# Optimization experiments

Measured on AMD Instinct MI355X. Metric: run time of the kernel, lower is better.

## Reference

```python
import jax, jax.numpy as jnp
import numpy as np

SIZE = 5   # local window side
HEADS = 1

def patch_extract(x, size):
    # x: [B, C, H, W] -> [B, C, size*size, H, W], replicate padding,
    # window index l = i*size + j (row-major over kernel), matching F.unfold.
    p = size // 2
    xp = jnp.pad(x, ((0, 0), (0, 0), (p, p), (p, p)), mode='edge')
    H, W = x.shape[2], x.shape[3]
    windows = [xp[:, :, i:i + H, j:j + W] for i in range(size) for j in range(size)]
    return jnp.stack(windows, axis=2)

def setup_inputs() -> dict:
    key = jax.random.key(0)
    k1, k2, k3, k4 = jax.random.split(key, 4)
    B, C, H, W = 4, 128, 64, 128
    attn = jax.random.normal(k1, (B, HEADS, H * W, SIZE * SIZE), dtype=jnp.float32)
    fmap = jax.random.normal(k2, (B, C, H, W), dtype=jnp.float32)
    Wv = jax.random.normal(k3, (C, C), dtype=jnp.float32) * (1.0 / np.sqrt(C))
    gamma = jax.random.normal(k4, (1,), dtype=jnp.float32)
    return {"attn": attn, "fmap": fmap, "Wv": Wv, "gamma": gamma}

def reference(attn, fmap, Wv, gamma):
    B, C, H, W = fmap.shape
    d = C // HEADS
    L = SIZE * SIZE
    # to_v: 1x1 conv, no bias
    v = jnp.einsum('oc,bchw->bohw', Wv, fmap)
    # local window gather: [B, C, L, H, W]
    v = patch_extract(v, SIZE)
    # 'b (h d) l x y -> b h (x y) d l'
    v = v.reshape(B, HEADS, d, L, H, W)
    v = v.transpose(0, 1, 4, 5, 2, 3).reshape(B, HEADS, H * W, d, L)
    # weighted sum over the local window
    out = jnp.einsum('bhnl,bhndl->bhnd', attn, v)
    # 'b h (x y) d -> b (h d) x y'
    out = out.reshape(B, HEADS, H, W, d).transpose(0, 1, 4, 2, 3).reshape(B, C, H, W)
    return fmap + gamma[0] * out
```

## Files before the change

kernel.cpp:

```cpp
#include <hip/hip_runtime.h>


namespace {
constexpr int Bn = 4, Cn = 128, Hn = 64, Wn = 128, Ln = 25;
constexpr int HWn = Hn * Wn;

constexpr int TY = 4, TX = 16;
constexpr int HY = 8, HX = 24;
constexpr int RS = 136;
constexpr int SVS = 136;
constexpr int WVS = 136;

typedef __attribute__((ext_vector_type(8))) short short8;
typedef __attribute__((ext_vector_type(4))) float f32x4;

__device__ inline unsigned short f2bf(float f) {
    unsigned u = __float_as_uint(f);
    return (unsigned short)((u + 0x7fffu + ((u >> 16) & 1u)) >> 16);
}

__global__ __launch_bounds__(256) void lsa_fused(
    const float* __restrict__ attn, const float* __restrict__ fmap,
    const float* __restrict__ Wv, const float* __restrict__ gamma,
    float* __restrict__ out)
{
    __shared__ alignas(16) unsigned short hs[HY * HX * RS];
    __shared__ alignas(16) unsigned short sv[TY * TX * SVS];
    __shared__ float at_s[TY * TX * Ln];

    const int tid = threadIdx.x;
    const int b = blockIdx.z;
    const int x0 = blockIdx.x * TX;
    const int y0 = blockIdx.y * TY;

    for (int i = tid; i < HY * 64 * 6; i += 256) {
        const int k = i % 6;
        const int r = i / 6;
        const int cp = r & 63;
        const int dy = r >> 6;
        const int ry = min(max(y0 + dy - 2, 0), Hn - 1);
        const int gxb = x0 - 4 + 4 * k;
        const size_t rowb = ((size_t)(b * Cn + 2 * cp)) * HWn + (size_t)ry * Wn;
        float4 va, vb;
        if (gxb < 0) {
            const float s0 = fmap[rowb], s1 = fmap[rowb + HWn];
            va.x = va.y = va.z = va.w = s0;
            vb.x = vb.y = vb.z = vb.w = s1;
        } else if (gxb > Wn - 4) {
            const float s0 = fmap[rowb + Wn - 1], s1 = fmap[rowb + HWn + Wn - 1];
            va.x = va.y = va.z = va.w = s0;
            vb.x = vb.y = vb.z = vb.w = s1;
        } else {
            va = *(const float4*)&fmap[rowb + gxb];
            vb = *(const float4*)&fmap[rowb + HWn + gxb];
        }
        unsigned short* hbase = &hs[(dy * HX + 4 * k) * RS + 2 * cp];
        *(unsigned*)&hbase[0 * RS] = (unsigned)f2bf(va.x) | ((unsigned)f2bf(vb.x) << 16);
        *(unsigned*)&hbase[1 * RS] = (unsigned)f2bf(va.y) | ((unsigned)f2bf(vb.y) << 16);
        *(unsigned*)&hbase[2 * RS] = (unsigned)f2bf(va.z) | ((unsigned)f2bf(vb.z) << 16);
        *(unsigned*)&hbase[3 * RS] = (unsigned)f2bf(va.w) | ((unsigned)f2bf(vb.w) << 16);
    }
    {
        const size_t ab = ((size_t)b * HWn + (size_t)y0 * Wn + x0) * Ln;
        for (int i = tid; i < TY * TX * Ln; i += 256) {
            const int yi = i / 400, j = i - yi * 400;
            at_s[i] = attn[ab + (size_t)yi * (Wn * Ln) + j];
        }
    }
    __syncthreads();

    const int xi = tid & 15, kq = (tid >> 4) & 3, yi = tid >> 6;
    const int p = yi * 16 + xi;
    float acc[32];
#pragma unroll
    for (int j = 0; j < 32; ++j) acc[j] = 0.f;

#pragma unroll
    for (int l = 0; l < Ln; ++l) {
        const int dy = l / 5, dx = l % 5;
        const float a = at_s[p * Ln + l];
        const unsigned short* row = &hs[((yi + dy) * HX + (2 + xi + dx)) * RS + kq * 32];
#pragma unroll
        for (int q = 0; q < 4; ++q) {
            uint4 u = *(const uint4*)&row[q * 8];
            const unsigned w[4] = {u.x, u.y, u.z, u.w};
#pragma unroll
            for (int e = 0; e < 4; ++e) {
                acc[q * 8 + 2 * e + 0] += a * __uint_as_float(w[e] << 16);
                acc[q * 8 + 2 * e + 1] += a * __uint_as_float(w[e] & 0xffff0000u);
            }
        }
    }
    {
        unsigned short* dst = &sv[p * SVS + kq * 32];
#pragma unroll
        for (int q = 0; q < 4; ++q) {
            unsigned pk[4];
#pragma unroll
            for (int e = 0; e < 4; ++e)
                pk[e] = (unsigned)f2bf(acc[q * 8 + 2 * e]) |
                        ((unsigned)f2bf(acc[q * 8 + 2 * e + 1]) << 16);
            uint4 v; v.x = pk[0]; v.y = pk[1]; v.z = pk[2]; v.w = pk[3];
            *(uint4*)&dst[q * 8] = v;
        }
    }
    float4 wq[16];
#pragma unroll
    for (int t = 0; t < 16; ++t)
        wq[t] = *(const float4*)&Wv[(size_t)(tid + t * 256) * 4];

    __syncthreads();

#pragma unroll
    for (int t = 0; t < 16; ++t) {
        const int i4 = tid + t * 256;
        const int r = i4 >> 5;
        const int c = (i4 & 31) * 4;
        uint2 v;
        v.x = (unsigned)f2bf(wq[t].x) | ((unsigned)f2bf(wq[t].y) << 16);
        v.y = (unsigned)f2bf(wq[t].z) | ((unsigned)f2bf(wq[t].w) << 16);
        *(uint2*)&hs[r * WVS + c] = v;
    }
    __syncthreads();

    const int wave = tid >> 6, lane = tid & 63;
    const int m16 = lane & 15, q = lane >> 4;
    const int n = (y0 + wave) * Wn + x0 + m16;
    const float g = gamma[0];

    short8 bfrag[4];
    {
        const unsigned short* srow = &sv[(wave * 16 + m16) * SVS + q * 8];
#pragma unroll
        for (int kk = 0; kk < 4; ++kk) bfrag[kk] = *(const short8*)(srow + kk * 32);
    }
    f32x4 accv[8];
#pragma unroll
    for (int t = 0; t < 8; ++t) { f32x4 z = {0.f, 0.f, 0.f, 0.f}; accv[t] = z; }

#pragma unroll
    for (int t = 0; t < 8; ++t) {
        const unsigned short* arow = &hs[(t * 16 + m16) * WVS + q * 8];
#pragma unroll
        for (int kk = 0; kk < 4; ++kk) {
            short8 af = *(const short8*)(arow + kk * 32);
            accv[t] = __builtin_amdgcn_mfma_f32_16x16x32_bf16(af, bfrag[kk], accv[t], 0, 0, 0);
        }
    }

#pragma unroll
    for (int t = 0; t < 8; ++t) {
#pragma unroll
        for (int r = 0; r < 4; ++r) {
            const int c = t * 16 + q * 4 + r;
            const size_t idx = ((size_t)(b * Cn + c)) * HWn + n;
            out[idx] = fmap[idx] + g * accv[t][r];
        }
    }
}
}

extern "C" void kernel_launch(void* const* d_in, const int* in_sizes, int n_in,
                              void* d_out, int out_size, void* d_ws, size_t ws_size,
                              hipStream_t stream) {
    const float* attn  = (const float*)d_in[0];
    const float* fmap  = (const float*)d_in[1];
    const float* Wv    = (const float*)d_in[2];
    const float* gamma = (const float*)d_in[3];
    float* out = (float*)d_out;

    dim3 grid(Wn / TX, Hn / TY, Bn);
    lsa_fused<<<grid, 256, 0, stream>>>(attn, fmap, Wv, gamma, out);
}
```

Baseline: 99.74 us.

## Double block size to 512 threads, splitting channel and output work finer

Raises the block to 512 threads. Each thread now accumulates 16 channels instead of 32 in the window-sum phase, and each wave computes half of the output channels in the MFMA projection phase. The Wv prefetch into registers that ran before the barrier is removed; Wv is now loaded and converted after the barrier. The aim is to cut per-thread register pressure and add more waves to hide latency, at the cost of more threads per block and a serialized Wv load.

```diff
diff --git a/kernel.cpp b/kernel.cpp
--- a/kernel.cpp
+++ b/kernel.cpp
@@ -10,6 +10,7 @@
 constexpr int RS = 136;
 constexpr int SVS = 136;
 constexpr int WVS = 136;
+constexpr int NT = 512;
 
 typedef __attribute__((ext_vector_type(8))) short short8;
 typedef __attribute__((ext_vector_type(4))) float f32x4;
@@ -19,7 +20,7 @@
     return (unsigned short)((u + 0x7fffu + ((u >> 16) & 1u)) >> 16);
 }
 
-__global__ __launch_bounds__(256) void lsa_fused(
+__global__ __launch_bounds__(NT, 4) void lsa_fused(
     const float* __restrict__ attn, const float* __restrict__ fmap,
     const float* __restrict__ Wv, const float* __restrict__ gamma,
     float* __restrict__ out)
@@ -33,7 +34,7 @@
     const int x0 = blockIdx.x * TX;
     const int y0 = blockIdx.y * TY;
 
-    for (int i = tid; i < HY * 64 * 6; i += 256) {
+    for (int i = tid; i < HY * 64 * 6; i += NT) {
         const int k = i % 6;
         const int r = i / 6;
         const int cp = r & 63;
@@ -62,26 +63,26 @@
     }
     {
         const size_t ab = ((size_t)b * HWn + (size_t)y0 * Wn + x0) * Ln;
-        for (int i = tid; i < TY * TX * Ln; i += 256) {
+        for (int i = tid; i < TY * TX * Ln; i += NT) {
             const int yi = i / 400, j = i - yi * 400;
             at_s[i] = attn[ab + (size_t)yi * (Wn * Ln) + j];
         }
     }
     __syncthreads();
 
-    const int xi = tid & 15, kq = (tid >> 4) & 3, yi = tid >> 6;
+    const int xi = tid & 15, kq = (tid >> 4) & 7, yi = tid >> 7;
     const int p = yi * 16 + xi;
-    float acc[32];
+    float acc[16];
 #pragma unroll
-    for (int j = 0; j < 32; ++j) acc[j] = 0.f;
+    for (int j = 0; j < 16; ++j) acc[j] = 0.f;
 
 #pragma unroll
     for (int l = 0; l < Ln; ++l) {
         const int dy = l / 5, dx = l % 5;
         const float a = at_s[p * Ln + l];
-        const unsigned short* row = &hs[((yi + dy) * HX + (2 + xi + dx)) * RS + kq * 32];
+        const unsigned short* row = &hs[((yi + dy) * HX + (2 + xi + dx)) * RS + kq * 16];
 #pragma unroll
-        for (int q = 0; q < 4; ++q) {
+        for (int q = 0; q < 2; ++q) {
             uint4 u = *(const uint4*)&row[q * 8];
             const unsigned w[4] = {u.x, u.y, u.z, u.w};
 #pragma unroll
@@ -92,9 +93,9 @@
         }
     }
     {
-        unsigned short* dst = &sv[p * SVS + kq * 32];
+        unsigned short* dst = &sv[p * SVS + kq * 16];
 #pragma unroll
-        for (int q = 0; q < 4; ++q) {
+        for (int q = 0; q < 2; ++q) {
             unsigned pk[4];
 #pragma unroll
             for (int e = 0; e < 4; ++e)
@@ -104,43 +105,42 @@
             *(uint4*)&dst[q * 8] = v;
         }
     }
-    float4 wq[16];
-#pragma unroll
-    for (int t = 0; t < 16; ++t)
-        wq[t] = *(const float4*)&Wv[(size_t)(tid + t * 256) * 4];
-
     __syncthreads();
 
 #pragma unroll
-    for (int t = 0; t < 16; ++t) {
-        const int i4 = tid + t * 256;
+    for (int t = 0; t < 8; ++t) {
+        const int i4 = tid + t * NT;
+        const float4 w = *(const float4*)&Wv[(size_t)i4 * 4];
         const int r = i4 >> 5;
         const int c = (i4 & 31) * 4;
         uint2 v;
-        v.x = (unsigned)f2bf(wq[t].x) | ((unsigned)f2bf(wq[t].y) << 16);
-        v.y = (unsigned)f2bf(wq[t].z) | ((unsigned)f2bf(wq[t].w) << 16);
+        v.x = (unsigned)f2bf(w.x) | ((unsigned)f2bf(w.y) << 16);
+        v.y = (unsigned)f2bf(w.z) | ((unsigned)f2bf(w.w) << 16);
         *(uint2*)&hs[r * WVS + c] = v;
     }
     __syncthreads();
 
     const int wave = tid >> 6, lane = tid & 63;
     const int m16 = lane & 15, q = lane >> 4;
-    const int n = (y0 + wave) * Wn + x0 + m16;
+    const int wrow = wave >> 1;
+    const int mhalf = wave & 1;
+    const int n = (y0 + wrow) * Wn + x0 + m16;
     const float g = gamma[0];
 
     short8 bfrag[4];
     {
-        const unsigned short* srow = &sv[(wave * 16 + m16) * SVS + q * 8];
+        const unsigned short* srow = &sv[(wrow * 16 + m16) * SVS + q * 8];
 #pragma unroll
         for (int kk = 0; kk < 4; ++kk) bfrag[kk] = *(const short8*)(srow + kk * 32);
     }
-    f32x4 accv[8];
+    f32x4 accv[4];
 #pragma unroll
-    for (int t = 0; t < 8; ++t) { f32x4 z = {0.f, 0.f, 0.f, 0.f}; accv[t] = z; }
+    for (int t = 0; t < 4; ++t) { f32x4 z = {0.f, 0.f, 0.f, 0.f}; accv[t] = z; }
 
 #pragma unroll
-    for (int t = 0; t < 8; ++t) {
-        const unsigned short* arow = &hs[(t * 16 + m16) * WVS + q * 8];
+    for (int t = 0; t < 4; ++t) {
+        const int mg = mhalf * 4 + t;
+        const unsigned short* arow = &hs[(mg * 16 + m16) * WVS + q * 8];
 #pragma unroll
         for (int kk = 0; kk < 4; ++kk) {
             short8 af = *(const short8*)(arow + kk * 32);
@@ -149,10 +149,11 @@
     }
 
 #pragma unroll
-    for (int t = 0; t < 8; ++t) {
+    for (int t = 0; t < 4; ++t) {
+        const int mg = mhalf * 4 + t;
 #pragma unroll
         for (int r = 0; r < 4; ++r) {
-            const int c = t * 16 + q * 4 + r;
+            const int c = mg * 16 + q * 4 + r;
             const size_t idx = ((size_t)(b * Cn + c)) * HWn + n;
             out[idx] = fmap[idx] + g * accv[t][r];
         }
@@ -170,5 +171,5 @@
     float* out = (float*)d_out;
 
     dim3 grid(Wn / TX, Hn / TY, Bn);
-    lsa_fused<<<grid, 256, 0, stream>>>(attn, fmap, Wv, gamma, out);
+    lsa_fused<<<grid, NT, 0, stream>>>(attn, fmap, Wv, gamma, out);
 }
```

After: 98.97 us. Within noise of the previous version (-0.8%).
